# Kernel tuning notes

Hardware: AMD Instinct MI355X
Metric: run time of the kernel (lower is better)

## Reference

```python
import jax, jax.numpy as jnp
import numpy as np

IN_F, OUT_F, NG = 2048, 8192, 16
EPS = 1e-5

def setup_inputs() -> dict:
    key = jax.random.key(0)
    k = jax.random.split(key, 6)
    x = jax.random.normal(k[0], (4096, IN_F), dtype=jnp.float32)
    W = jax.random.normal(k[1], (OUT_F, IN_F), dtype=jnp.float32) * (1.0 / np.sqrt(IN_F))
    b = jax.random.normal(k[2], (OUT_F,), dtype=jnp.float32) * 0.01
    gn_w = jnp.ones((OUT_F,), dtype=jnp.float32)
    gn_b = jnp.zeros((OUT_F,), dtype=jnp.float32)
    mult_w = jax.random.normal(k[3], (OUT_F,), dtype=jnp.float32)
    return {"x": x, "W": W, "b": b, "gn_w": gn_w, "gn_b": gn_b, "mult_w": mult_w}

def reference(x, W, b, gn_w, gn_b, mult_w):
    B = x.shape[0]
    y = x @ W.T + b  # [B, OUT_F]
    g = y.reshape(B, NG, OUT_F // NG)
    mean = jnp.mean(g, axis=-1, keepdims=True)
    var = jnp.mean(jnp.square(g - mean), axis=-1, keepdims=True)
    n = ((g - mean) * jax.lax.rsqrt(var + EPS)).reshape(B, OUT_F)
    n = n * gn_w + gn_b
    s1 = n * jax.nn.sigmoid(n)
    m = s1 * mult_w
    return m * jax.nn.sigmoid(m)
```

## Files before the change

### kernel.cpp

```cpp
#include <hip/hip_runtime.h>

#define M_DIM 4096
#define N_DIM 8192
#define K_DIM 2048
#define NGRP 16
#define GSZ 512
#define EPSV 1e-5f

#define NX (M_DIM * K_DIM)
#define NW (N_DIM * K_DIM)
#define NY ((size_t)M_DIM * N_DIM)

typedef __attribute__((ext_vector_type(8))) short bf16x8;
typedef __attribute__((ext_vector_type(4))) float f32x4;
typedef __attribute__((ext_vector_type(8))) short shortx8;

__device__ __forceinline__ float b2f(short u) {
    union { unsigned u32; float f; } c;
    c.u32 = ((unsigned)(unsigned short)u) << 16;
    return c.f;
}

__device__ __forceinline__ short f2b(float f) {
    union { float f; unsigned u; } c; c.f = f;
    unsigned r = (c.u + 0x7fffu + ((c.u >> 16) & 1u)) >> 16;
    return (short)r;
}

__global__ __launch_bounds__(256) void convert_kernel(
    const float* __restrict__ x, const float* __restrict__ W,
    short* __restrict__ dst)
{
    const size_t base = ((size_t)blockIdx.x * 256 + threadIdx.x) * 32;
    const float* src = (base < NX) ? (x + base) : (W + (base - NX));
    f32x4 v[8];
#pragma unroll
    for (int c = 0; c < 8; ++c) v[c] = *(const f32x4*)(src + c * 4);
#pragma unroll
    for (int c = 0; c < 4; ++c) {
        shortx8 o;
#pragma unroll
        for (int j = 0; j < 4; ++j) {
            o[j]     = f2b(v[2 * c][j]);
            o[j + 4] = f2b(v[2 * c + 1][j]);
        }
        *(shortx8*)(dst + base + c * 8) = o;
    }
}

__global__ __launch_bounds__(256) void gemm_bt_bf16_kernel(
    const short* __restrict__ A, const short* __restrict__ W, short* __restrict__ C)
{
    __shared__ __align__(16) short ldsA[128 * 32];
    __shared__ __align__(16) short ldsB[128 * 32];

    const int tid  = threadIdx.x;
    const int lane = tid & 63;
    const int wave = tid >> 6;
    const int blockRow = blockIdx.y * 128;
    const int blockCol = blockIdx.x * 128;

    const int sub = lane >> 2;
    const int kq  = (((lane & 3) ^ ((lane >> 3) & 3))) * 8;

    const int wm  = (wave >> 1) * 64;
    const int wn  = (wave & 1) * 64;
    const int fr  = lane & 15;
    const int fko = (((lane >> 4) ^ ((fr >> 1) & 3))) * 8;

    f32x4 acc[4][4] = {};

    for (int k0 = 0; k0 < K_DIM; k0 += 32) {
#pragma unroll
        for (int c = 0; c < 4; ++c) {
            const int chunk = wave * 4 + c;
            const int j = chunk & 7;
            const int row = j * 16 + sub;
            const short* g;
            short* l;
            if (chunk < 8) {
                g = A + (size_t)(blockRow + row) * K_DIM + k0 + kq;
                l = ldsA + j * 512;
            } else {
                g = W + (size_t)(blockCol + row) * K_DIM + k0 + kq;
                l = ldsB + j * 512;
            }
            __builtin_amdgcn_global_load_lds(
                (const __attribute__((address_space(1))) void*)g,
                (__attribute__((address_space(3))) void*)l,
                16, 0, 0);
        }
        __syncthreads();

        bf16x8 af[4], bfv[4];
#pragma unroll
        for (int i = 0; i < 4; ++i) {
            af[i]  = *(const bf16x8*)(ldsA + (wm + i * 16 + fr) * 32 + fko);
            bfv[i] = *(const bf16x8*)(ldsB + (wn + i * 16 + fr) * 32 + fko);
        }
#pragma unroll
        for (int i = 0; i < 4; ++i)
#pragma unroll
            for (int j = 0; j < 4; ++j)
                acc[i][j] = __builtin_amdgcn_mfma_f32_16x16x32_bf16(
                    af[i], bfv[j], acc[i][j], 0, 0, 0);
        __syncthreads();
    }

    const int er = (lane >> 4) * 4;
    const int ec = lane & 15;
#pragma unroll
    for (int i = 0; i < 4; ++i) {
        const int r0 = blockRow + wm + i * 16 + er;
#pragma unroll
        for (int j = 0; j < 4; ++j) {
            const int c0 = blockCol + wn + j * 16 + ec;
#pragma unroll
            for (int r = 0; r < 4; ++r)
                C[(size_t)(r0 + r) * N_DIM + c0] = f2b(acc[i][j][r]);
        }
    }
}

__global__ __launch_bounds__(256) void gn_silu_bf16_kernel(
    const short* __restrict__ Y,
    const float* __restrict__ bias,
    const float* __restrict__ gnw,
    const float* __restrict__ gnb,
    const float* __restrict__ mw,
    float* __restrict__ out)
{
    const int lane = threadIdx.x & 63;
    const int wave = threadIdx.x >> 6;
    const unsigned gid = blockIdx.x * 4u + wave;
    const unsigned row = gid >> 4;
    const unsigned grp = gid & 15;
    const int col = grp * GSZ + lane * 8;
    const size_t off = (size_t)row * N_DIM + col;

    bf16x8 v = *(const bf16x8*)(Y + off);
    f32x4 b0 = *(const f32x4*)(bias + col);
    f32x4 b1 = *(const f32x4*)(bias + col + 4);

    float y[8];
    float s = 0.f, s2 = 0.f;
#pragma unroll
    for (int j = 0; j < 8; ++j) {
        y[j] = b2f(v[j]) + (j < 4 ? b0[j] : b1[j - 4]);
        s  += y[j];
        s2 += y[j] * y[j];
    }
#pragma unroll
    for (int d = 1; d < 64; d <<= 1) {
        s  += __shfl_xor(s,  d, 64);
        s2 += __shfl_xor(s2, d, 64);
    }
    const float mean = s * (1.0f / GSZ);
    const float var  = s2 * (1.0f / GSZ) - mean * mean;
    const float inv  = rsqrtf(var + EPSV);

    f32x4 w0 = *(const f32x4*)(gnw + col);
    f32x4 w1 = *(const f32x4*)(gnw + col + 4);
    f32x4 g0 = *(const f32x4*)(gnb + col);
    f32x4 g1 = *(const f32x4*)(gnb + col + 4);
    f32x4 m0 = *(const f32x4*)(mw + col);
    f32x4 m1 = *(const f32x4*)(mw + col + 4);

    f32x4 o0, o1;
#pragma unroll
    for (int j = 0; j < 8; ++j) {
        float gwv = j < 4 ? w0[j] : w1[j - 4];
        float gbv = j < 4 ? g0[j] : g1[j - 4];
        float mwv = j < 4 ? m0[j] : m1[j - 4];
        float n  = (y[j] - mean) * inv * gwv + gbv;
        float s1 = n / (1.f + __expf(-n));
        float m  = s1 * mwv;
        float r  = m / (1.f + __expf(-m));
        if (j < 4) o0[j] = r; else o1[j - 4] = r;
    }
    *(f32x4*)(out + off)     = o0;
    *(f32x4*)(out + off + 4) = o1;
}

__global__ __launch_bounds__(256) void gemm_bt_f32_kernel(
    const float* __restrict__ A, const float* __restrict__ W, float* __restrict__ C)
{
    __shared__ __align__(16) short ldsA[128 * 32];
    __shared__ __align__(16) short ldsB[128 * 32];

    const int tid  = threadIdx.x;
    const int lane = tid & 63;
    const int wave = tid >> 6;
    const int blockRow = blockIdx.y * 128;
    const int blockCol = blockIdx.x * 128;
    const int srow = tid >> 1;
    const int scol = (tid & 1) * 16;
    const int wm  = (wave >> 1) * 64;
    const int wn  = (wave & 1) * 64;
    const int fr  = lane & 15;
    const int fko = (lane >> 4) * 8;

    f32x4 acc[4][4] = {};
    const size_t aRowOff = (size_t)(blockRow + srow) * K_DIM;
    const size_t wRowOff = (size_t)(blockCol + srow) * K_DIM;

    for (int k0 = 0; k0 < K_DIM; k0 += 32) {
        f32x4 va0 = *(const f32x4*)(A + aRowOff + k0 + scol);
        f32x4 va1 = *(const f32x4*)(A + aRowOff + k0 + scol + 4);
        f32x4 va2 = *(const f32x4*)(A + aRowOff + k0 + scol + 8);
        f32x4 va3 = *(const f32x4*)(A + aRowOff + k0 + scol + 12);
        f32x4 vb0 = *(const f32x4*)(W + wRowOff + k0 + scol);
        f32x4 vb1 = *(const f32x4*)(W + wRowOff + k0 + scol + 4);
        f32x4 vb2 = *(const f32x4*)(W + wRowOff + k0 + scol + 8);
        f32x4 vb3 = *(const f32x4*)(W + wRowOff + k0 + scol + 12);
        bf16x8 a0, a1, b0, b1;
#pragma unroll
        for (int j = 0; j < 4; ++j) {
            a0[j] = f2b(va0[j]); a0[j + 4] = f2b(va1[j]);
            a1[j] = f2b(va2[j]); a1[j + 4] = f2b(va3[j]);
            b0[j] = f2b(vb0[j]); b0[j + 4] = f2b(vb1[j]);
            b1[j] = f2b(vb2[j]); b1[j + 4] = f2b(vb3[j]);
        }
        *(bf16x8*)(ldsA + srow * 32 + scol)     = a0;
        *(bf16x8*)(ldsA + srow * 32 + scol + 8) = a1;
        *(bf16x8*)(ldsB + srow * 32 + scol)     = b0;
        *(bf16x8*)(ldsB + srow * 32 + scol + 8) = b1;
        __syncthreads();

        bf16x8 af[4], bfv[4];
#pragma unroll
        for (int i = 0; i < 4; ++i) {
            af[i]  = *(const bf16x8*)(ldsA + (wm + i * 16 + fr) * 32 + fko);
            bfv[i] = *(const bf16x8*)(ldsB + (wn + i * 16 + fr) * 32 + fko);
        }
#pragma unroll
        for (int i = 0; i < 4; ++i)
#pragma unroll
            for (int j = 0; j < 4; ++j)
                acc[i][j] = __builtin_amdgcn_mfma_f32_16x16x32_bf16(
                    af[i], bfv[j], acc[i][j], 0, 0, 0);
        __syncthreads();
    }

    const int er = (lane >> 4) * 4;
    const int ec = lane & 15;
#pragma unroll
    for (int i = 0; i < 4; ++i) {
        const int r0 = blockRow + wm + i * 16 + er;
#pragma unroll
        for (int j = 0; j < 4; ++j) {
            const int c0 = blockCol + wn + j * 16 + ec;
#pragma unroll
            for (int r = 0; r < 4; ++r)
                C[(size_t)(r0 + r) * N_DIM + c0] = acc[i][j][r];
        }
    }
}

__global__ __launch_bounds__(256) void gn_silu_f32_kernel(
    float* __restrict__ Y,
    const float* __restrict__ bias,
    const float* __restrict__ gnw,
    const float* __restrict__ gnb,
    const float* __restrict__ mw)
{
    const int lane = threadIdx.x & 63;
    const int wave = threadIdx.x >> 6;
    const unsigned gid = blockIdx.x * 4u + wave;
    const unsigned row = gid >> 4;
    const unsigned grp = gid & 15;
    const int col = grp * GSZ + lane * 8;
    const size_t off = (size_t)row * N_DIM + col;

    f32x4 v0 = *(const f32x4*)(Y + off);
    f32x4 v1 = *(const f32x4*)(Y + off + 4);
    f32x4 b0 = *(const f32x4*)(bias + col);
    f32x4 b1 = *(const f32x4*)(bias + col + 4);

    float y[8];
    float s = 0.f, s2 = 0.f;
#pragma unroll
    for (int j = 0; j < 8; ++j) {
        y[j] = (j < 4 ? v0[j] + b0[j] : v1[j - 4] + b1[j - 4]);
        s += y[j]; s2 += y[j] * y[j];
    }
#pragma unroll
    for (int d = 1; d < 64; d <<= 1) {
        s  += __shfl_xor(s,  d, 64);
        s2 += __shfl_xor(s2, d, 64);
    }
    const float mean = s * (1.0f / GSZ);
    const float var  = s2 * (1.0f / GSZ) - mean * mean;
    const float inv  = rsqrtf(var + EPSV);

    f32x4 w0 = *(const f32x4*)(gnw + col);
    f32x4 w1 = *(const f32x4*)(gnw + col + 4);
    f32x4 g0 = *(const f32x4*)(gnb + col);
    f32x4 g1 = *(const f32x4*)(gnb + col + 4);
    f32x4 m0 = *(const f32x4*)(mw + col);
    f32x4 m1 = *(const f32x4*)(mw + col + 4);

    f32x4 o0, o1;
#pragma unroll
    for (int j = 0; j < 8; ++j) {
        float gwv = j < 4 ? w0[j] : w1[j - 4];
        float gbv = j < 4 ? g0[j] : g1[j - 4];
        float mwv = j < 4 ? m0[j] : m1[j - 4];
        float n  = (y[j] - mean) * inv * gwv + gbv;
        float s1 = n / (1.f + __expf(-n));
        float m  = s1 * mwv;
        float r  = m / (1.f + __expf(-m));
        if (j < 4) o0[j] = r; else o1[j - 4] = r;
    }
    *(f32x4*)(Y + off)     = o0;
    *(f32x4*)(Y + off + 4) = o1;
}

extern "C" void kernel_launch(void* const* d_in, const int* in_sizes, int n_in,
                              void* d_out, int out_size, void* d_ws, size_t ws_size,
                              hipStream_t stream)
{
    const float* x   = (const float*)d_in[0];
    const float* W   = (const float*)d_in[1];
    const float* b   = (const float*)d_in[2];
    const float* gnw = (const float*)d_in[3];
    const float* gnb = (const float*)d_in[4];
    const float* mw  = (const float*)d_in[5];
    float* out = (float*)d_out;

    const size_t need = ((size_t)NX + NW + NY) * sizeof(short);
    dim3 ggrid(N_DIM / 128, M_DIM / 128);
    const int ngroups = M_DIM * NGRP;

    if (ws_size >= need) {
        short* xb = (short*)d_ws;
        short* Wb = xb + NX;
        short* yb = Wb + NW;

        convert_kernel<<<(NX + NW) / (256 * 32), 256, 0, stream>>>(x, W, xb);
        gemm_bt_bf16_kernel<<<ggrid, 256, 0, stream>>>(xb, Wb, yb);
        gn_silu_bf16_kernel<<<ngroups / 4, 256, 0, stream>>>(yb, b, gnw, gnb, mw, out);
    } else {
        gemm_bt_f32_kernel<<<ggrid, 256, 0, stream>>>(x, W, out);
        gn_silu_f32_kernel<<<ngroups / 4, 256, 0, stream>>>(out, b, gnw, gnb, mw);
    }
}
```

Measured before the change: 401.3 us.

## Use 256x256 GEMM tiles with a 4-stage LDS prefetch pipeline

Replaces the 128x128, single-buffered bf16 GEMM with a 256x256-tile kernel using 512 threads (8 waves, each owning a 128x64 sub-tile). It keeps four LDS buffers and issues global_load_lds three tiles ahead, using explicit vmcnt waits and barriers, so memory latency overlaps with MFMA work. MFMA sections also get raised wave priority. The larger tile cuts global traffic per flop. The 128KB of LDS and larger accumulator arrays lower occupancy, and the schedule relies on hand-tuned waitcnt counts.

```diff
diff --git a/kernel.cpp b/kernel.cpp
--- a/kernel.cpp
+++ b/kernel.cpp
@@ -48,76 +48,104 @@
     }
 }
 
-__global__ __launch_bounds__(256) void gemm_bt_bf16_kernel(
+#define BKS 32
+#define NTILES (K_DIM / BKS)
+
+__global__ __launch_bounds__(512, 2) void gemm256_bf16_kernel(
     const short* __restrict__ A, const short* __restrict__ W, short* __restrict__ C)
 {
-    __shared__ __align__(16) short ldsA[128 * 32];
-    __shared__ __align__(16) short ldsB[128 * 32];
+    __shared__ __align__(16) short lds[4 * 16384];
 
     const int tid  = threadIdx.x;
     const int lane = tid & 63;
     const int wave = tid >> 6;
-    const int blockRow = blockIdx.y * 128;
-    const int blockCol = blockIdx.x * 128;
-
-    const int sub = lane >> 2;
-    const int kq  = (((lane & 3) ^ ((lane >> 3) & 3))) * 8;
-
-    const int wm  = (wave >> 1) * 64;
-    const int wn  = (wave & 1) * 64;
-    const int fr  = lane & 15;
-    const int fko = (((lane >> 4) ^ ((fr >> 1) & 3))) * 8;
-
-    f32x4 acc[4][4] = {};
-
-    for (int k0 = 0; k0 < K_DIM; k0 += 32) {
-#pragma unroll
-        for (int c = 0; c < 4; ++c) {
-            const int chunk = wave * 4 + c;
-            const int j = chunk & 7;
-            const int row = j * 16 + sub;
-            const short* g;
-            short* l;
-            if (chunk < 8) {
-                g = A + (size_t)(blockRow + row) * K_DIM + k0 + kq;
-                l = ldsA + j * 512;
-            } else {
-                g = W + (size_t)(blockCol + row) * K_DIM + k0 + kq;
-                l = ldsB + j * 512;
-            }
-            __builtin_amdgcn_global_load_lds(
-                (const __attribute__((address_space(1))) void*)g,
-                (__attribute__((address_space(3))) void*)l,
-                16, 0, 0);
-        }
-        __syncthreads();
-
-        bf16x8 af[4], bfv[4];
-#pragma unroll
-        for (int i = 0; i < 4; ++i) {
-            af[i]  = *(const bf16x8*)(ldsA + (wm + i * 16 + fr) * 32 + fko);
-            bfv[i] = *(const bf16x8*)(ldsB + (wn + i * 16 + fr) * 32 + fko);
-        }
-#pragma unroll
-        for (int i = 0; i < 4; ++i)
+    const int wr   = wave >> 2;
+    const int wc   = wave & 3;
+    const int blockRow = blockIdx.y * 256;
+    const int blockCol = blockIdx.x * 256;
+
+    const int q0 = tid, q1 = tid + 512;
+    const int sr0 = q0 >> 2, sc0 = (q0 & 3) ^ (sr0 & 3);
+    const int sr1 = q1 >> 2, sc1 = (q1 & 3) ^ (sr1 & 3);
+    const short* gA0 = A + (size_t)(blockRow + sr0) * K_DIM + sc0 * 8;
+    const short* gA1 = A + (size_t)(blockRow + sr1) * K_DIM + sc1 * 8;
+    const short* gB0 = W + (size_t)(blockCol + sr0) * K_DIM + sc0 * 8;
+    const short* gB1 = W + (size_t)(blockCol + sr1) * K_DIM + sc1 * 8;
+
+    const int fr    = lane & 15;
+    const int pbyte = ((lane >> 4) ^ (fr & 3)) * 16;
+    const int aBase = (wr * 128 + fr) * 64 + pbyte;
+    const int bBase = (wc * 64  + fr) * 64 + pbyte;
+
+    f32x4 acc[8][4] = {};
+
+    auto stageT = [&](int t) {
+        short* dA = lds + (t & 3) * 16384;
+        short* dB = dA + 8192;
+        const int ko = t * BKS;
+        __builtin_amdgcn_global_load_lds(
+            (const __attribute__((address_space(1))) void*)(gA0 + ko),
+            (__attribute__((address_space(3))) void*)(dA + q0 * 8), 16, 0, 0);
+        __builtin_amdgcn_global_load_lds(
+            (const __attribute__((address_space(1))) void*)(gB0 + ko),
+            (__attribute__((address_space(3))) void*)(dB + q0 * 8), 16, 0, 0);
+        __builtin_amdgcn_global_load_lds(
+            (const __attribute__((address_space(1))) void*)(gA1 + ko),
+            (__attribute__((address_space(3))) void*)(dA + q1 * 8), 16, 0, 0);
+        __builtin_amdgcn_global_load_lds(
+            (const __attribute__((address_space(1))) void*)(gB1 + ko),
+            (__attribute__((address_space(3))) void*)(dB + q1 * 8), 16, 0, 0);
+    };
+
+    stageT(0); stageT(1); stageT(2);
+
+    for (int t = 0; t < NTILES; ++t) {
+        __builtin_amdgcn_s_barrier();
+        __builtin_amdgcn_sched_barrier(0);
+        if (t + 3 < NTILES) {
+            stageT(t + 3);
+            asm volatile("s_waitcnt vmcnt(12)" ::: "memory");
+        } else if (t + 2 < NTILES) {
+            asm volatile("s_waitcnt vmcnt(8)" ::: "memory");
+        } else if (t + 1 < NTILES) {
+            asm volatile("s_waitcnt vmcnt(4)" ::: "memory");
+        } else {
+            asm volatile("s_waitcnt vmcnt(0)" ::: "memory");
+        }
+        __builtin_amdgcn_s_barrier();
+        __builtin_amdgcn_sched_barrier(0);
+
+        const char* bufA = (const char*)lds + (t & 3) * 32768;
+        const char* bufB = bufA + 16384;
+        bf16x8 af[8], bfv[4];
+#pragma unroll
+        for (int i = 0; i < 8; ++i)
+            af[i] = *(const bf16x8*)(bufA + aBase + i * 1024);
+#pragma unroll
+        for (int j = 0; j < 4; ++j)
+            bfv[j] = *(const bf16x8*)(bufB + bBase + j * 1024);
+
+        __builtin_amdgcn_s_setprio(1);
+#pragma unroll
+        for (int i = 0; i < 8; ++i)
 #pragma unroll
             for (int j = 0; j < 4; ++j)
                 acc[i][j] = __builtin_amdgcn_mfma_f32_16x16x32_bf16(
                     af[i], bfv[j], acc[i][j], 0, 0, 0);
-        __syncthreads();
+        __builtin_amdgcn_s_setprio(0);
     }
 
     const int er = (lane >> 4) * 4;
     const int ec = lane & 15;
 #pragma unroll
-    for (int i = 0; i < 4; ++i) {
-        const int r0 = blockRow + wm + i * 16 + er;
+    for (int i = 0; i < 8; ++i) {
+        const int rr = blockRow + wr * 128 + i * 16 + er;
 #pragma unroll
         for (int j = 0; j < 4; ++j) {
-            const int c0 = blockCol + wn + j * 16 + ec;
+            const int cc = blockCol + wc * 64 + j * 16 + ec;
 #pragma unroll
             for (int r = 0; r < 4; ++r)
-                C[(size_t)(r0 + r) * N_DIM + c0] = f2b(acc[i][j][r]);
+                C[(size_t)(rr + r) * N_DIM + cc] = f2b(acc[i][j][r]);
         }
     }
 }
@@ -329,7 +357,6 @@
     float* out = (float*)d_out;
 
     const size_t need = ((size_t)NX + NW + NY) * sizeof(short);
-    dim3 ggrid(N_DIM / 128, M_DIM / 128);
     const int ngroups = M_DIM * NGRP;
 
     if (ws_size >= need) {
@@ -338,9 +365,11 @@
         short* yb = Wb + NW;
 
         convert_kernel<<<(NX + NW) / (256 * 32), 256, 0, stream>>>(x, W, xb);
-        gemm_bt_bf16_kernel<<<ggrid, 256, 0, stream>>>(xb, Wb, yb);
+        dim3 g256(N_DIM / 256, M_DIM / 256);
+        gemm256_bf16_kernel<<<g256, 512, 0, stream>>>(xb, Wb, yb);
         gn_silu_bf16_kernel<<<ngroups / 4, 256, 0, stream>>>(yb, b, gnw, gnb, mw, out);
     } else {
+        dim3 ggrid(N_DIM / 128, M_DIM / 128);
         gemm_bt_f32_kernel<<<ggrid, 256, 0, stream>>>(x, W, out);
         gn_silu_f32_kernel<<<ngroups / 4, 256, 0, stream>>>(out, b, gnw, gnb, mw);
     }
```

Result: faster. 381.4 us (-5.0%).
